# Performance work log

Measured on AMD Instinct MI355X. Metric: run time of the kernel, lower is better.

## Reference

```python
import jax, jax.numpy as jnp
import numpy as np

SAMPLE_RATE = 16000
N_TRANSIENTS = 20
TRANSIENT_SAMPLES = 1600  # int(0.1 s * 16000 Hz)
BATCH = 64
MAX_TRANSIENTS = 256
AUDIO_LEN = 160000  # 10 s @ 16 kHz


def setup_inputs() -> dict:
    key = jax.random.key(0)
    k1, k2, k3, k4 = jax.random.split(key, 4)
    # timings in seconds, sorted per batch (as in generate_random_transients)
    transient_timings = jnp.sort(
        jax.random.uniform(k1, (BATCH, MAX_TRANSIENTS), dtype=jnp.float32) * 9.0, axis=1)
    transient_ids = jax.random.randint(k2, (BATCH, MAX_TRANSIENTS), 0, N_TRANSIENTS)
    transient_gains = 0.1 + 0.9 * jax.random.uniform(k3, (BATCH, MAX_TRANSIENTS), dtype=jnp.float32)
    transient_templates = jax.random.normal(k4, (N_TRANSIENTS, TRANSIENT_SAMPLES), dtype=jnp.float32)
    return {
        "transient_timings": transient_timings,
        "transient_ids": transient_ids,
        "transient_gains": transient_gains,
        "transient_templates": transient_templates,
        "audio_length": AUDIO_LEN,
    }


def reference(transient_timings, transient_ids, transient_gains, transient_templates, audio_length):
    n_tr, L = transient_templates.shape
    # start sample of each transient (timings are non-negative, so floor == int())
    t_sample = jnp.floor(transient_timings * SAMPLE_RATE).astype(jnp.int32)  # [B, T]
    # skip conditions from the original loop: gain <= 0, id >= n_transients, start >= audio_length
    valid = (transient_gains > 0) & (transient_ids < n_tr) & (t_sample < audio_length)
    # gather templates: [B, T, L]
    tmpl = transient_templates[jnp.clip(transient_ids, 0, n_tr - 1)]
    vals = tmpl * (transient_gains * valid.astype(transient_gains.dtype))[..., None]
    # destination positions: [B, T, L]; positions >= audio_length are dropped (truncation)
    pos = t_sample[..., None] + jnp.arange(L, dtype=jnp.int32)

    def scatter_one(p, v):
        # p, v: [T, L] -> scatter-add into [audio_length]
        return jnp.zeros((audio_length,), v.dtype).at[p.reshape(-1)].add(
            v.reshape(-1), mode='drop')

    return jax.vmap(scatter_one)(pos, vals)  # [B, audio_length]
```

## Files before the change

kernel.cpp:

```cpp
#include <hip/hip_runtime.h>


constexpr int SR    = 16000;
constexpr int TL    = 1600;
constexpr int MAXT  = 256;
constexpr int NTHR  = 256;
constexpr int CHUNK = 1024;

__global__ __launch_bounds__(NTHR)
void transient_gather(const float* __restrict__ timings,
                      const int*   __restrict__ ids,
                      const float* __restrict__ gains,
                      const float* __restrict__ templates,
                      float*       __restrict__ out,
                      int T, int n_tr, int A)
{
    __shared__ int2               s_m[MAXT];
    __shared__ unsigned long long s_mask[NTHR / 64];

    const int b      = blockIdx.y;
    const int chunk0 = blockIdx.x * CHUNK;
    const int tid    = (int)threadIdx.x;

    {
        const float tm = timings[(size_t)b * T + tid];
        const float g  = gains  [(size_t)b * T + tid];
        const int   id = ids    [(size_t)b * T + tid];
        const int   ts = (int)floorf(tm * (float)SR);
        const bool ok  = (g > 0.0f) & (id < n_tr) & (ts < A);
        const int tsc  = min(max(ts, 0), A);
        const int idc  = min(max(id, 0), n_tr - 1);
        s_m[tid] = make_int2((tsc << 8) | idc, ok ? __float_as_int(g) : 0);

        const bool ov = (tsc < chunk0 + CHUNK) && (tsc + TL > chunk0);
        const unsigned long long m = __ballot(ov);
        if ((tid & 63) == 0) s_mask[tid >> 6] = m;
    }
    __syncthreads();

    int lo = T, hi = -1;
#pragma unroll
    for (int w = 0; w < NTHR / 64; ++w) {
        const unsigned long long mw = s_mask[w];
        if (mw) {
            lo = min(lo, w * 64 + (int)__builtin_ctzll(mw));
            hi = max(hi, w * 64 + 63 - (int)__builtin_clzll(mw));
        }
    }

    float acc[4] = {0.f, 0.f, 0.f, 0.f};
    const int off_base = chunk0 + tid;

    for (int j = lo; j <= hi; ++j) {
        const int2  m  = s_m[j];
        const int   ts = m.x >> 8;
        const float g  = __int_as_float(m.y);
        const float* __restrict__ row = templates + (size_t)(m.x & 255) * TL;
        const int off0 = off_base - ts;
#pragma unroll
        for (int k = 0; k < 4; ++k) {
            const int o = off0 + k * NTHR;
            if ((unsigned)o < (unsigned)TL)
                acc[k] += g * row[o];
        }
    }

    float* ob = out + (size_t)b * A + off_base;
#pragma unroll
    for (int k = 0; k < 4; ++k) {
        if (off_base + k * NTHR < A)
            __builtin_nontemporal_store(acc[k], &ob[k * NTHR]);
    }
}

extern "C" void kernel_launch(void* const* d_in, const int* in_sizes, int n_in,
                              void* d_out, int out_size, void* d_ws, size_t ws_size,
                              hipStream_t stream) {
    const float* timings   = (const float*)d_in[0];
    const int*   ids       = (const int*)  d_in[1];
    const float* gains     = (const float*)d_in[2];
    const float* templates = (const float*)d_in[3];
    float*       out       = (float*)d_out;

    const int T    = MAXT;
    const int B    = in_sizes[0] / T;
    const int n_tr = in_sizes[3] / TL;
    const int A    = out_size / B;

    dim3 grid((A + CHUNK - 1) / CHUNK, B), block(NTHR);
    transient_gather<<<grid, block, 0, stream>>>(timings, ids, gains, templates, out,
                                                 T, n_tr, A);
}
```

Measured before the change: 24.98 us.

## Use grid-stride chunk loop per batch row to amortize metadata setup

Changes the grid from one block per chunk to a fixed 32 blocks per batch row. Each block loads the transient metadata once, then loops over several chunks, recomputing the overlap range with per-chunk ballots. It also makes the per-transient metadata wave-uniform with readfirstlane and skips zero-gain entries. The aim is to cut the repeated metadata loads and the block launch overhead, at the cost of fewer blocks (2048 instead of about 10k) and serial work inside each block.

```diff
diff --git a/kernel.cpp b/kernel.cpp
--- a/kernel.cpp
+++ b/kernel.cpp
@@ -6,21 +6,22 @@
 constexpr int MAXT  = 256;
 constexpr int NTHR  = 256;
 constexpr int CHUNK = 1024;
+constexpr int BPB   = 32;
 
-__global__ __launch_bounds__(NTHR)
-void transient_gather(const float* __restrict__ timings,
-                      const int*   __restrict__ ids,
-                      const float* __restrict__ gains,
-                      const float* __restrict__ templates,
-                      float*       __restrict__ out,
-                      int T, int n_tr, int A)
+__global__ __launch_bounds__(NTHR, 8)
+void transient_gs(const float* __restrict__ timings,
+                  const int*   __restrict__ ids,
+                  const float* __restrict__ gains,
+                  const float* __restrict__ templates,
+                  float*       __restrict__ out,
+                  int T, int n_tr, int A, int nchunk)
 {
-    __shared__ int2               s_m[MAXT];
-    __shared__ unsigned long long s_mask[NTHR / 64];
+    __shared__ int2 s_m [MAXT];
+    __shared__ int  s_ts[MAXT];
 
-    const int b      = blockIdx.y;
-    const int chunk0 = blockIdx.x * CHUNK;
-    const int tid    = (int)threadIdx.x;
+    const int b    = blockIdx.y;
+    const int tid  = (int)threadIdx.x;
+    const int lane = tid & 63;
 
     {
         const float tm = timings[(size_t)b * T + tid];
@@ -30,46 +31,55 @@
         const bool ok  = (g > 0.0f) & (id < n_tr) & (ts < A);
         const int tsc  = min(max(ts, 0), A);
         const int idc  = min(max(id, 0), n_tr - 1);
-        s_m[tid] = make_int2((tsc << 8) | idc, ok ? __float_as_int(g) : 0);
-
-        const bool ov = (tsc < chunk0 + CHUNK) && (tsc + TL > chunk0);
-        const unsigned long long m = __ballot(ov);
-        if ((tid & 63) == 0) s_mask[tid >> 6] = m;
+        s_m [tid] = make_int2((tsc << 8) | idc, ok ? __float_as_int(g) : 0);
+        s_ts[tid] = tsc;
     }
     __syncthreads();
 
-    int lo = T, hi = -1;
+    int tsr[4];
 #pragma unroll
-    for (int w = 0; w < NTHR / 64; ++w) {
-        const unsigned long long mw = s_mask[w];
-        if (mw) {
-            lo = min(lo, w * 64 + (int)__builtin_ctzll(mw));
-            hi = max(hi, w * 64 + 63 - (int)__builtin_clzll(mw));
+    for (int q = 0; q < 4; ++q) tsr[q] = s_ts[q * 64 + lane];
+
+    for (int c = blockIdx.x; c < nchunk; c += BPB) {
+        const int chunk0 = c * CHUNK;
+
+        int lo = T, hi = -1;
+#pragma unroll
+        for (int q = 0; q < 4; ++q) {
+            const bool ov = (tsr[q] < chunk0 + CHUNK) & (tsr[q] + TL > chunk0);
+            const unsigned long long m = __ballot(ov);
+            if (m) {
+                lo = min(lo, q * 64 + (int)__builtin_ctzll(m));
+                hi = max(hi, q * 64 + 63 - (int)__builtin_clzll(m));
+            }
         }
-    }
 
-    float acc[4] = {0.f, 0.f, 0.f, 0.f};
-    const int off_base = chunk0 + tid;
+        float acc[4] = {0.f, 0.f, 0.f, 0.f};
+        const int off_base = chunk0 + tid;
 
-    for (int j = lo; j <= hi; ++j) {
-        const int2  m  = s_m[j];
-        const int   ts = m.x >> 8;
-        const float g  = __int_as_float(m.y);
-        const float* __restrict__ row = templates + (size_t)(m.x & 255) * TL;
-        const int off0 = off_base - ts;
+        for (int j = lo; j <= hi; ++j) {
+            const int2 mj  = s_m[j];
+            const int  mx  = __builtin_amdgcn_readfirstlane(mj.x);
+            const int  mgb = __builtin_amdgcn_readfirstlane(mj.y);
+            if (mgb == 0) continue;
+            const float g  = __int_as_float(mgb);
+            const int   ts = mx >> 8;
+            const float* __restrict__ row = templates + (size_t)(mx & 255) * TL;
+            const int off0 = off_base - ts;
+#pragma unroll
+            for (int k = 0; k < 4; ++k) {
+                const int o = off0 + k * NTHR;
+                if ((unsigned)o < (unsigned)TL)
+                    acc[k] += g * row[o];
+            }
+        }
+
+        float* ob = out + (size_t)b * A + off_base;
 #pragma unroll
         for (int k = 0; k < 4; ++k) {
-            const int o = off0 + k * NTHR;
-            if ((unsigned)o < (unsigned)TL)
-                acc[k] += g * row[o];
+            if (off_base + k * NTHR < A)
+                __builtin_nontemporal_store(acc[k], &ob[k * NTHR]);
         }
-    }
-
-    float* ob = out + (size_t)b * A + off_base;
-#pragma unroll
-    for (int k = 0; k < 4; ++k) {
-        if (off_base + k * NTHR < A)
-            __builtin_nontemporal_store(acc[k], &ob[k * NTHR]);
     }
 }
 
@@ -82,12 +92,13 @@
     const float* templates = (const float*)d_in[3];
     float*       out       = (float*)d_out;
 
-    const int T    = MAXT;
-    const int B    = in_sizes[0] / T;
-    const int n_tr = in_sizes[3] / TL;
-    const int A    = out_size / B;
+    const int T      = MAXT;
+    const int B      = in_sizes[0] / T;
+    const int n_tr   = in_sizes[3] / TL;
+    const int A      = out_size / B;
+    const int nchunk = (A + CHUNK - 1) / CHUNK;
 
-    dim3 grid((A + CHUNK - 1) / CHUNK, B), block(NTHR);
-    transient_gather<<<grid, block, 0, stream>>>(timings, ids, gains, templates, out,
-                                                 T, n_tr, A);
+    dim3 grid(BPB, B), block(NTHR);
+    transient_gs<<<grid, block, 0, stream>>>(timings, ids, gains, templates, out,
+                                             T, n_tr, A, nchunk);
 }
```

After: 27.67 us. +10.8%, slower.
